# Kernel tuning notes

Hardware: AMD Instinct MI355X
Metric: run time of the kernel (lower is better)

Reference implementation:

```python
import jax, jax.numpy as jnp
import numpy as np

B, T, D, A = 64, 1024, 768, 128

def setup_inputs() -> dict:
    key = jax.random.key(0)
    k1, k2, k3 = jax.random.split(key, 3)
    x = jax.random.normal(k1, (B, T, D), dtype=jnp.float32)
    # glorot_normal-style scaling for the learned projections
    W1 = jax.random.normal(k2, (D, A), dtype=jnp.float32) * np.sqrt(2.0 / (D + A))
    W2 = jax.random.normal(k3, (A, T), dtype=jnp.float32) * np.sqrt(2.0 / (A + T))
    return {"x": x, "W1": W1, "W2": W2}

def reference(x, W1, W2):
    # x: [B, T, D], W1: [D, A], W2: [A, T]
    OA = jnp.tanh(jnp.einsum('btd,da->bta', x, W1))      # [B, T, A]
    OA = jnp.einsum('bta,as->bts', OA, W2)               # [B, T, T]
    OA = jax.nn.softmax(OA, axis=-2)                     # softmax over source-time axis
    # ot[b,s,d] = sum_t x[b,t,d] * OA[b,t,s]  (x^T @ OA, then transpose back)
    ot = jnp.einsum('btd,bts->bsd', x, OA)               # [B, T, D]
    return ot
```

## Files before the change

### kernel.cpp

```cpp
#include <hip/hip_runtime.h>
#include <math.h>

#define B_ 64
#define T_ 1024
#define D_ 768
#define A_ 128

typedef __attribute__((ext_vector_type(4))) float f32x4;
typedef __attribute__((ext_vector_type(8))) short s16x8;
typedef __attribute__((ext_vector_type(4))) short s16x4;

__device__ inline short f2b(float f) {
  union { float f; unsigned u; } v; v.f = f;
  unsigned r = (v.u + 0x7FFFu + ((v.u >> 16) & 1u)) >> 16;
  return (short)r;
}
__device__ inline float b2f(short s) {
  union { unsigned u; float f; } v; v.u = ((unsigned)(unsigned short)s) << 16;
  return v.f;
}

__device__ inline void gll16(const void* g, const void* lds) {
  __builtin_amdgcn_global_load_lds(
      (const __attribute__((address_space(1))) unsigned*)g,
      (__attribute__((address_space(3))) unsigned*)lds, 16, 0, 0);
}

__global__ __launch_bounds__(512, 2)
void g4_div(const short* __restrict__ Ag, const short* __restrict__ Bg,
            const float* __restrict__ Rs, float* __restrict__ Cg) {
  __shared__ __align__(16) short AS[2][16384];
  __shared__ __align__(16) short BS[2][16384];
  unsigned nwg = gridDim.x;
  unsigned L = blockIdx.x;
  unsigned xcd = L & 7u, base = L >> 3;
  unsigned q = nwg >> 3, r = nwg & 7u;
  unsigned id = (xcd < r ? xcd * (q + 1) : r * (q + 1) + (xcd - r) * q) + base;
  const int bz = id / 12;
  const int rem = id - bz * 12;
  const int by = rem / 3, bx = rem - (rem / 3) * 3;
  const int m0 = by * 256, n0 = bx * 256;

  const short* Ab = Ag + (size_t)bz * (T_ * T_);
  const short* Bb = Bg + (size_t)bz * (D_ * T_);
  const float* rsb = Rs + (size_t)bz * T_;
  float* Cb = Cg + (size_t)bz * (T_ * D_);

  const int tid = threadIdx.x;
  const int w = tid >> 6, lane = tid & 63;
  const int wr = w >> 2, wc = w & 3;
  const int lr = lane & 15, lq = lane >> 4;
  const int swzk = (lane & 7) ^ ((lane >> 3) & 7);
  const int abase = (wr * 128 + lr) * 64;
  const int bbase = (wc * 64 + lr) * 64;
  const int sx = lr & 7;
  const int sl0 = (lq ^ sx) * 8;
  const int sl1 = ((4 + lq) ^ sx) * 8;

  f32x4 acc[8][4] = {};
  s16x8 bq[4][2];

#define STG(dst, src, r0, kt)                                                  \
  { _Pragma("unroll")                                                          \
    for (int jj = 0; jj < 2; ++jj) {                                           \
      int rr = jj * 64 + w * 8 + (lane >> 3);                                  \
      gll16((src) + (size_t)((r0) + rr) * 1024 + (kt) + swzk * 8,              \
            (dst) + jj * 4096 + w * 512);                                      \
    } }

#define PH2(P, Q0, VM, ...)                                                    \
  {                                                                            \
    s16x8 a0_ = *(const s16x8*)&AS[P][abase + (2 * (Q0)) * 1024 + sl0];        \
    s16x8 a1_ = *(const s16x8*)&AS[P][abase + (2 * (Q0)) * 1024 + sl1];        \
    s16x8 a2_ = *(const s16x8*)&AS[P][abase + (2 * (Q0) + 1) * 1024 + sl0];    \
    s16x8 a3_ = *(const s16x8*)&AS[P][abase + (2 * (Q0) + 1) * 1024 + sl1];    \
    if ((Q0) == 0) {                                                           \
      _Pragma("unroll")                                                        \
      for (int nf = 0; nf < 4; ++nf) {                                         \
        bq[nf][0] = *(const s16x8*)&BS[P][bbase + nf * 1024 + sl0];            \
        bq[nf][1] = *(const s16x8*)&BS[P][bbase + nf * 1024 + sl1];            \
      }                                                                        \
    }                                                                          \
    __VA_ARGS__;                                                               \
    VM;                                                                        \
    __builtin_amdgcn_s_barrier();                                              \
    asm volatile("s_waitcnt lgkmcnt(0)" ::: "memory");                         \
    __builtin_amdgcn_s_setprio(1);                                             \
    _Pragma("unroll")                                                          \
    for (int nf = 0; nf < 4; ++nf) {                                           \
      acc[2*(Q0)][nf]   = __builtin_amdgcn_mfma_f32_16x16x32_bf16(a0_, bq[nf][0], acc[2*(Q0)][nf], 0, 0, 0);   \
      acc[2*(Q0)+1][nf] = __builtin_amdgcn_mfma_f32_16x16x32_bf16(a2_, bq[nf][0], acc[2*(Q0)+1][nf], 0, 0, 0); \
    }                                                                          \
    s16x8 a4_ = *(const s16x8*)&AS[P][abase + (2 * (Q0) + 2) * 1024 + sl0];    \
    s16x8 a5_ = *(const s16x8*)&AS[P][abase + (2 * (Q0) + 2) * 1024 + sl1];    \
    s16x8 a6_ = *(const s16x8*)&AS[P][abase + (2 * (Q0) + 3) * 1024 + sl0];    \
    s16x8 a7_ = *(const s16x8*)&AS[P][abase + (2 * (Q0) + 3) * 1024 + sl1];    \
    _Pragma("unroll")                                                          \
    for (int nf = 0; nf < 4; ++nf) {                                           \
      acc[2*(Q0)][nf]   = __builtin_amdgcn_mfma_f32_16x16x32_bf16(a1_, bq[nf][1], acc[2*(Q0)][nf], 0, 0, 0);   \
      acc[2*(Q0)+1][nf] = __builtin_amdgcn_mfma_f32_16x16x32_bf16(a3_, bq[nf][1], acc[2*(Q0)+1][nf], 0, 0, 0); \
    }                                                                          \
    _Pragma("unroll")                                                          \
    for (int nf = 0; nf < 4; ++nf) {                                           \
      acc[2*(Q0)+2][nf] = __builtin_amdgcn_mfma_f32_16x16x32_bf16(a4_, bq[nf][0], acc[2*(Q0)+2][nf], 0, 0, 0); \
      acc[2*(Q0)+3][nf] = __builtin_amdgcn_mfma_f32_16x16x32_bf16(a6_, bq[nf][0], acc[2*(Q0)+3][nf], 0, 0, 0); \
    }                                                                          \
    _Pragma("unroll")                                                          \
    for (int nf = 0; nf < 4; ++nf) {                                           \
      acc[2*(Q0)+2][nf] = __builtin_amdgcn_mfma_f32_16x16x32_bf16(a5_, bq[nf][1], acc[2*(Q0)+2][nf], 0, 0, 0); \
      acc[2*(Q0)+3][nf] = __builtin_amdgcn_mfma_f32_16x16x32_bf16(a7_, bq[nf][1], acc[2*(Q0)+3][nf], 0, 0, 0); \
    }                                                                          \
    __builtin_amdgcn_s_setprio(0);                                             \
    __builtin_amdgcn_s_barrier();                                              \
  }

#define VM4 asm volatile("s_waitcnt vmcnt(4)" ::: "memory")
#define VM0 asm volatile("s_waitcnt vmcnt(0)" ::: "memory")
#define NOP (void)0

  STG(&BS[0][0],    Bb, n0,       0);
  STG(&BS[0][8192], Bb, n0 + 128, 0);
  STG(&AS[0][0],    Ab, m0,       0);
  STG(&AS[0][8192], Ab, m0 + 128, 0);
  STG(&BS[1][0],    Bb, n0,       64);
  STG(&BS[1][8192], Bb, n0 + 128, 64);
  VM4;
  __builtin_amdgcn_s_barrier();

  for (int j = 0; j < 7; ++j) {
    const int kb = j * 128;
    PH2(0, 0, NOP,
        STG(&AS[1][0],    Ab, m0,       kb + 64);
        STG(&AS[1][8192], Ab, m0 + 128, kb + 64));
    PH2(0, 2, VM4,
        STG(&BS[0][0],    Bb, n0,       kb + 128);
        STG(&BS[0][8192], Bb, n0 + 128, kb + 128));
    PH2(1, 0, NOP,
        STG(&AS[0][0],    Ab, m0,       kb + 128);
        STG(&AS[0][8192], Ab, m0 + 128, kb + 128));
    PH2(1, 2, VM4,
        STG(&BS[1][0],    Bb, n0,       kb + 192);
        STG(&BS[1][8192], Bb, n0 + 128, kb + 192));
  }
  PH2(0, 0, NOP,
      STG(&AS[1][0],    Ab, m0,       960);
      STG(&AS[1][8192], Ab, m0 + 128, 960));
  PH2(0, 2, VM0, NOP);
  PH2(1, 0, NOP, NOP);
  PH2(1, 2, NOP, NOP);

#undef STG
#undef PH2
#undef VM4
#undef VM0
#undef NOP

#pragma unroll
  for (int mf = 0; mf < 8; ++mf) {
    f32x4 rsv = *(const f32x4*)&rsb[m0 + wr * 128 + mf * 16 + lq * 4];
    f32x4 inv;
#pragma unroll
    for (int qq = 0; qq < 4; ++qq) {
      float iv;
      asm("v_rcp_f32 %0, %1" : "=v"(iv) : "v"(rsv[qq]));
      inv[qq] = iv;
    }
#pragma unroll
    for (int nf = 0; nf < 4; ++nf) {
      int m = m0 + wr * 128 + mf * 16 + lq * 4;
      int n = n0 + wc * 64 + nf * 16 + lr;
#pragma unroll
      for (int qq = 0; qq < 4; ++qq)
        Cb[(size_t)(m + qq) * D_ + n] = acc[mf][nf][qq] * inv[qq];
    }
  }
}

__global__ __launch_bounds__(256, 2)
void g12(const short* __restrict__ W1tg, const float* __restrict__ xg,
         const short* __restrict__ W2tg, short* __restrict__ Stg,
         float* __restrict__ rsg, short* __restrict__ xtg, int nb) {
  __shared__ __align__(16) short SMEM[33792];
  short* As = SMEM;
  short* Bs = SMEM + 8192;
  short* Ts = SMEM + 16384;
  short* Hs = SMEM;
  short* B2 = SMEM + 16384;

  unsigned nwg = gridDim.x;
  unsigned L = blockIdx.x;
  unsigned xcd = L & 7u, base = L >> 3;
  unsigned q = nwg >> 3, r = nwg & 7u;
  unsigned id = (xcd < r ? xcd * (q + 1) : r * (q + 1) + (xcd - r) * q) + base;
  const int bz = id >> 3, bt = id & 7;
  const int t0 = bt * 128;

  const float* xb = xg + (size_t)bz * T_ * D_;
  short* Xtb = xtg + (size_t)bz * ((size_t)D_ * T_);
  short* Stb = Stg + (size_t)bz * (T_ * T_);
  float* rsb = rsg + (size_t)bz * T_;

  const int tid = threadIdx.x;
  const int w = tid >> 6, lane = tid & 63;
  const int wr = w >> 1, wc = w & 1;
  const int lr = lane & 15, lq = lane >> 4;
  const int r8 = lane >> 3, c8 = lane & 7;

  f32x4 acc[4][4] = {};

  for (int k0 = 0; k0 < D_; k0 += 64) {
    __syncthreads();
#pragma unroll
    for (int i = 0; i < 4; ++i) {
      int chunk = w * 4 + i;
      int row = chunk * 8 + r8;
      gll16(W1tg + (size_t)row * D_ + k0 + c8 * 8, As + chunk * 512);
    }
    s16x8 parr[4];
#pragma unroll
    for (int u = 0; u < 4; ++u) {
      int c = tid * 4 + u;
      int row = c >> 3, k8 = c & 7;
      const float* gp = xb + (size_t)(t0 + row) * D_ + k0 + k8 * 8;
      float4 f0 = *(const float4*)gp;
      float4 f1 = *(const float4*)(gp + 4);
      s16x8 p;
      p[0] = f2b(f0.x); p[1] = f2b(f0.y); p[2] = f2b(f0.z); p[3] = f2b(f0.w);
      p[4] = f2b(f1.x); p[5] = f2b(f1.y); p[6] = f2b(f1.z); p[7] = f2b(f1.w);
      parr[u] = p;
      *(s16x8*)&Bs[row * 64 + k8 * 8] = p;
    }
    __syncthreads();
#pragma unroll
    for (int kk = 0; kk < 2; ++kk) {
      s16x8 a[4], b[4];
#pragma unroll
      for (int mf = 0; mf < 4; ++mf)
        a[mf] = *(const s16x8*)&As[(wr * 64 + mf * 16 + lr) * 64 + kk * 32 + lq * 8];
#pragma unroll
      for (int nf = 0; nf < 4; ++nf)
        b[nf] = *(const s16x8*)&Bs[(wc * 64 + nf * 16 + lr) * 64 + kk * 32 + lq * 8];
#pragma unroll
      for (int mf = 0; mf < 4; ++mf)
#pragma unroll
        for (int nf = 0; nf < 4; ++nf)
          acc[mf][nf] = __builtin_amdgcn_mfma_f32_16x16x32_bf16(
              a[mf], b[nf], acc[mf][nf], 0, 0, 0);
    }
#pragma unroll
    for (int u = 0; u < 4; ++u) {
      int c = tid * 4 + u;
      int row = c >> 3, k8 = c & 7;
#pragma unroll
      for (int j = 0; j < 8; ++j) Ts[(k8 * 8 + j) * 136 + row] = parr[u][j];
    }
    __syncthreads();
#pragma unroll
    for (int u = 0; u < 4; ++u) {
      int task = tid + u * 256;
      int dd = task >> 4, t8 = task & 15;
      *(s16x8*)&Xtb[(size_t)(k0 + dd) * T_ + t0 + t8 * 8] =
          *(const s16x8*)&Ts[dd * 136 + t8 * 8];
    }
  }

  __syncthreads();
#pragma unroll
  for (int mf = 0; mf < 4; ++mf)
#pragma unroll
    for (int nf = 0; nf < 4; ++nf) {
      int ml = wr * 64 + mf * 16 + lq * 4;
      int nl = wc * 64 + nf * 16 + lr;
      s16x4 pk;
#pragma unroll
      for (int qq = 0; qq < 4; ++qq) pk[qq] = f2b(tanhf(acc[mf][nf][qq]));
      int slot = (ml >> 3) ^ (nl & 7);
      *(s16x4*)&Hs[nl * 128 + (slot << 3) + (ml & 7)] = pk;
    }
  __syncthreads();

  const int sxl = lr & 7;
  for (int si = 0; si < 8; ++si) {
    const int s0 = si * 128;
#pragma unroll
    for (int u = 0; u < 8; ++u) {
      int idx = tid + u * 256;
      int row = idx >> 4, c16 = idx & 15;
      *(s16x8*)&B2[row * 128 + ((c16 ^ (row & 7)) << 3)] =
          *(const s16x8*)&W2tg[(size_t)(s0 + row) * A_ + c16 * 8];
    }
    __syncthreads();
    f32x4 ac2[4][4] = {};
#pragma unroll
    for (int kk = 0; kk < 4; ++kk) {
      s16x8 a[4], b[4];
#pragma unroll
      for (int mf = 0; mf < 4; ++mf) {
        int row = wr * 64 + mf * 16 + lr;
        a[mf] = *(const s16x8*)&Hs[row * 128 + (((kk * 4 + lq) ^ sxl) << 3)];
      }
#pragma unroll
      for (int nf = 0; nf < 4; ++nf) {
        int row = wc * 64 + nf * 16 + lr;
        b[nf] = *(const s16x8*)&B2[row * 128 + (((kk * 4 + lq) ^ sxl) << 3)];
      }
#pragma unroll
      for (int mf = 0; mf < 4; ++mf)
#pragma unroll
        for (int nf = 0; nf < 4; ++nf)
          ac2[mf][nf] = __builtin_amdgcn_mfma_f32_16x16x32_bf16(
              a[mf], b[nf], ac2[mf][nf], 0, 0, 0);
    }
    __syncthreads();
    float psum[4] = {0.f, 0.f, 0.f, 0.f};
#pragma unroll
    for (int mf = 0; mf < 4; ++mf)
#pragma unroll
      for (int nf = 0; nf < 4; ++nf) {
        int ml = wr * 64 + mf * 16 + lq * 4;
        int nl = wc * 64 + nf * 16 + lr;
        s16x4 pk;
#pragma unroll
        for (int qq = 0; qq < 4; ++qq) {
          float v = __expf(ac2[mf][nf][qq]);
          pk[qq] = f2b(v);
          psum[nf] += b2f(pk[qq]);
        }
        *(s16x4*)&B2[nl * 136 + ml] = pk;
      }
#pragma unroll
    for (int nf = 0; nf < 4; ++nf) {
      psum[nf] += __shfl_xor(psum[nf], 16);
      psum[nf] += __shfl_xor(psum[nf], 32);
    }
    if (lq == 0) {
#pragma unroll
      for (int nf = 0; nf < 4; ++nf)
        atomicAdd(&rsb[s0 + wc * 64 + nf * 16 + lr], psum[nf]);
    }
    __syncthreads();
#pragma unroll
    for (int it = 0; it < 8; ++it) {
      int row = it * 16 + (tid >> 4);
      int col = (tid & 15) * 8;
      *(s16x8*)&Stb[(size_t)(s0 + row) * T_ + t0 + col] =
          *(const s16x8*)&B2[row * 136 + col];
    }
    __syncthreads();
  }
}

__global__ __launch_bounds__(256)
void transpose_cvt(const float* __restrict__ src, short* __restrict__ dst,
                   int R, int C) {
  __shared__ float sh[64][65];
  const int tid = threadIdx.x;
  const float* s = src + (size_t)blockIdx.z * R * C;
  short* d = dst + (size_t)blockIdx.z * R * C;
  const int r0 = blockIdx.y * 64, c0 = blockIdx.x * 64;
#pragma unroll
  for (int u = 0; u < 4; ++u) {
    int e = tid + u * 256;
    int rr = e >> 4, cc4 = (e & 15) * 4;
    float4 v = *(const float4*)&s[(size_t)(r0 + rr) * C + c0 + cc4];
    sh[rr][cc4 + 0] = v.x;
    sh[rr][cc4 + 1] = v.y;
    sh[rr][cc4 + 2] = v.z;
    sh[rr][cc4 + 3] = v.w;
  }
  __syncthreads();
#pragma unroll
  for (int u = 0; u < 4; ++u) {
    int e = tid + u * 256;
    int dr = e >> 4, tc4 = (e & 15) * 4;
    s16x4 pk;
#pragma unroll
    for (int j = 0; j < 4; ++j) pk[j] = f2b(sh[tc4 + j][dr]);
    *(s16x4*)&d[(size_t)(c0 + dr) * R + r0 + tc4] = pk;
  }
}

extern "C" void kernel_launch(void* const* d_in, const int* in_sizes, int n_in,
                              void* d_out, int out_size, void* d_ws, size_t ws_size,
                              hipStream_t stream) {
  const float* x  = (const float*)d_in[0];
  const float* W1 = (const float*)d_in[1];
  const float* W2 = (const float*)d_in[2];
  float* out = (float*)d_out;

  short* xt  = (short*)d_ws;
  short* W1t = xt + (size_t)B_ * D_ * T_;
  short* W2t = W1t + (size_t)A_ * D_;
  float* rs  = (float*)(W2t + (size_t)T_ * A_);
  short* St  = (short*)(rs + (size_t)B_ * T_);
  size_t fixed_bytes = (size_t)((char*)St - (char*)xt);
  long avail = (long)ws_size - (long)fixed_bytes;
  long per_b = (long)T_ * T_ * sizeof(short);
  int chunk = (int)(avail > 0 ? avail / per_b : 0);
  if (chunk > B_) chunk = B_;
  if (chunk < 1) chunk = 1;

  hipMemsetAsync(rs, 0, (size_t)B_ * T_ * sizeof(float), stream);

  transpose_cvt<<<dim3(A_ / 64, D_ / 64, 1), 256, 0, stream>>>(W1, W1t, D_, A_);
  transpose_cvt<<<dim3(T_ / 64, A_ / 64, 1), 256, 0, stream>>>(W2, W2t, A_, T_);

  for (int b0 = 0; b0 < B_; b0 += chunk) {
    int nb = B_ - b0; if (nb > chunk) nb = chunk;
    g12<<<8 * nb, 256, 0, stream>>>(
        W1t, x + (size_t)b0 * T_ * D_, W2t, St,
        rs + (size_t)b0 * T_, xt + (size_t)b0 * (size_t)D_ * T_, nb);
    g4_div<<<12 * nb, 512, 0, stream>>>(
        St, xt + (size_t)b0 * (size_t)D_ * T_, rs + (size_t)b0 * T_,
        out + (size_t)b0 * (size_t)T_ * D_);
  }
}
```

Measured before the change: 256.7 us.

## Prefetch x registers, swizzle LDS tiles, and async-load W2 tiles

The first GEMM stage now prefetches the next x tile into registers while MFMAs run on the current one. The As, Bs and Ts LDS tiles get XOR swizzles to avoid bank conflicts, and one barrier is dropped by writing the transposed tile together with the B tile. W2 tile loads in the second stage use global_load_lds with swizzled source addresses instead of going through registers. This adds register pressure from the prefetch buffers and relies on the swizzle being consistent between the writers and readers of each tile.

```diff
diff --git a/kernel.cpp b/kernel.cpp
--- a/kernel.cpp
+++ b/kernel.cpp
@@ -204,42 +204,68 @@
   const int w = tid >> 6, lane = tid & 63;
   const int wr = w >> 1, wc = w & 1;
   const int lr = lane & 15, lq = lane >> 4;
-  const int r8 = lane >> 3, c8 = lane & 7;
+  const int swzk = (lane & 7) ^ ((lane >> 3) & 7);
+  const int sxl = lr & 7;
+  const int sl0 = (lq ^ sxl) * 8;
+  const int sl1 = ((4 + lq) ^ sxl) * 8;
 
   f32x4 acc[4][4] = {};
 
+  float4 xf0[4], xf1[4];
+#pragma unroll
+  for (int u = 0; u < 4; ++u) {
+    int c = tid * 4 + u;
+    int row = c >> 3, k8 = c & 7;
+    const float* gp = xb + (size_t)(t0 + row) * D_ + k8 * 8;
+    xf0[u] = *(const float4*)gp;
+    xf1[u] = *(const float4*)(gp + 4);
+  }
+
   for (int k0 = 0; k0 < D_; k0 += 64) {
     __syncthreads();
-#pragma unroll
-    for (int i = 0; i < 4; ++i) {
-      int chunk = w * 4 + i;
-      int row = chunk * 8 + r8;
-      gll16(W1tg + (size_t)row * D_ + k0 + c8 * 8, As + chunk * 512);
-    }
-    s16x8 parr[4];
 #pragma unroll
     for (int u = 0; u < 4; ++u) {
       int c = tid * 4 + u;
       int row = c >> 3, k8 = c & 7;
-      const float* gp = xb + (size_t)(t0 + row) * D_ + k0 + k8 * 8;
-      float4 f0 = *(const float4*)gp;
-      float4 f1 = *(const float4*)(gp + 4);
       s16x8 p;
-      p[0] = f2b(f0.x); p[1] = f2b(f0.y); p[2] = f2b(f0.z); p[3] = f2b(f0.w);
-      p[4] = f2b(f1.x); p[5] = f2b(f1.y); p[6] = f2b(f1.z); p[7] = f2b(f1.w);
-      parr[u] = p;
-      *(s16x8*)&Bs[row * 64 + k8 * 8] = p;
-    }
-    __syncthreads();
+      p[0] = f2b(xf0[u].x); p[1] = f2b(xf0[u].y);
+      p[2] = f2b(xf0[u].z); p[3] = f2b(xf0[u].w);
+      p[4] = f2b(xf1[u].x); p[5] = f2b(xf1[u].y);
+      p[6] = f2b(xf1[u].z); p[7] = f2b(xf1[u].w);
+      *(s16x8*)&Bs[row * 64 + ((k8 ^ (row & 7)) << 3)] = p;
+#pragma unroll
+      for (int j = 0; j < 8; ++j) {
+        int d = k8 * 8 + j;
+        Ts[d * 136 + (row ^ (d & 32))] = p[j];
+      }
+    }
+#pragma unroll
+    for (int i = 0; i < 4; ++i) {
+      int chunk = w * 4 + i;
+      int row = chunk * 8 + (lane >> 3);
+      gll16(W1tg + (size_t)row * D_ + k0 + swzk * 8, As + chunk * 512);
+    }
+    __syncthreads();
+    if (k0 + 64 < D_) {
+#pragma unroll
+      for (int u = 0; u < 4; ++u) {
+        int c = tid * 4 + u;
+        int row = c >> 3, k8 = c & 7;
+        const float* gp = xb + (size_t)(t0 + row) * D_ + (k0 + 64) + k8 * 8;
+        xf0[u] = *(const float4*)gp;
+        xf1[u] = *(const float4*)(gp + 4);
+      }
+    }
 #pragma unroll
     for (int kk = 0; kk < 2; ++kk) {
+      const int sl = kk ? sl1 : sl0;
       s16x8 a[4], b[4];
 #pragma unroll
       for (int mf = 0; mf < 4; ++mf)
-        a[mf] = *(const s16x8*)&As[(wr * 64 + mf * 16 + lr) * 64 + kk * 32 + lq * 8];
+        a[mf] = *(const s16x8*)&As[(wr * 64 + mf * 16 + lr) * 64 + sl];
 #pragma unroll
       for (int nf = 0; nf < 4; ++nf)
-        b[nf] = *(const s16x8*)&Bs[(wc * 64 + nf * 16 + lr) * 64 + kk * 32 + lq * 8];
+        b[nf] = *(const s16x8*)&Bs[(wc * 64 + nf * 16 + lr) * 64 + sl];
 #pragma unroll
       for (int mf = 0; mf < 4; ++mf)
 #pragma unroll
@@ -247,20 +273,12 @@
           acc[mf][nf] = __builtin_amdgcn_mfma_f32_16x16x32_bf16(
               a[mf], b[nf], acc[mf][nf], 0, 0, 0);
     }
-#pragma unroll
-    for (int u = 0; u < 4; ++u) {
-      int c = tid * 4 + u;
-      int row = c >> 3, k8 = c & 7;
-#pragma unroll
-      for (int j = 0; j < 8; ++j) Ts[(k8 * 8 + j) * 136 + row] = parr[u][j];
-    }
-    __syncthreads();
 #pragma unroll
     for (int u = 0; u < 4; ++u) {
       int task = tid + u * 256;
       int dd = task >> 4, t8 = task & 15;
       *(s16x8*)&Xtb[(size_t)(k0 + dd) * T_ + t0 + t8 * 8] =
-          *(const s16x8*)&Ts[dd * 136 + t8 * 8];
+          *(const s16x8*)&Ts[dd * 136 + ((t8 ^ ((dd >> 3) & 4)) << 3)];
     }
   }
 
@@ -279,15 +297,14 @@
     }
   __syncthreads();
 
-  const int sxl = lr & 7;
   for (int si = 0; si < 8; ++si) {
     const int s0 = si * 128;
 #pragma unroll
-    for (int u = 0; u < 8; ++u) {
-      int idx = tid + u * 256;
-      int row = idx >> 4, c16 = idx & 15;
-      *(s16x8*)&B2[row * 128 + ((c16 ^ (row & 7)) << 3)] =
-          *(const s16x8*)&W2tg[(size_t)(s0 + row) * A_ + c16 * 8];
+    for (int i = 0; i < 8; ++i) {
+      int c = w * 8 + i;
+      int row = 4 * c + (lane >> 4);
+      gll16(W2tg + (size_t)(s0 + row) * A_ + (((lane & 15) ^ (row & 7)) << 3),
+            B2 + c * 512);
     }
     __syncthreads();
     f32x4 ac2[4][4] = {};
```

Result: no change. 252.6 us (-1.6%).
